# Optimization experiments

Measured on AMD Instinct MI355X. Metric: run time of the kernel, lower is better.

Reference implementation:

```python
import jax, jax.numpy as jnp
import numpy as np

TAU = 0.05       # sinkhorn temperature (functools.partial in GCN_Net)
SK_ITERS = 20    # sinkhorn max_iter


def _mlp(x, w1, b1, w2, b2):
    # nn.Sequential(Linear, ReLU, Linear)
    return jnp.maximum(x @ w1 + b1, 0.0) @ w2 + b2


def _cosine(f1, f2, eps=1e-8):
    # torch CosineSimilarity over broadcast (E1,1,D) x (1,E2,D), computed as a GEMM
    n1 = jnp.maximum(jnp.linalg.norm(f1, axis=-1), eps)
    n2 = jnp.maximum(jnp.linalg.norm(f2, axis=-1), eps)
    return (f1 @ f2.T) / (n1[:, None] * n2[None, :])


def _sinkhorn(s):
    # log-domain sinkhorn, alternating row/col normalization (pygmtools-style)
    log_s = s / TAU
    for i in range(SK_ITERS):
        log_s = log_s - jax.nn.logsumexp(log_s, axis=(1 if i % 2 == 0 else 0), keepdims=True)
    return jnp.exp(log_s)


def _build_conn_edges(preds):
    # fully-connected off-diagonal graph; edge feats [dx, dy, dist, cls_src, cls_dst]
    n = preds.shape[0]
    pos = preds[:, 1:3]
    cls = preds[:, 6]
    idx = np.arange(n)
    r, c = np.meshgrid(idx, idx, indexing='ij')
    m = r != c
    conn = np.stack([r[m], c[m]], axis=1)  # (E,2), static under jit
    src, dst = conn[:, 0], conn[:, 1]
    d = pos[dst] - pos[src]                             # (E,2)
    dist = jnp.linalg.norm(d, axis=-1, keepdims=True)   # (E,1)
    edges = jnp.concatenate([d, dist, cls[src][:, None], cls[dst][:, None]], axis=-1)  # (E,5)
    return jnp.asarray(conn), edges


def _forward(ego_preds, cav_preds, node_w1, node_b1, node_w2, node_b2,
             edge_w1, edge_b1, edge_w2, edge_b2,
             l0_self_w, l0_self_b, l0_conv_w, l0_conv_b, l0_cls_w, l0_cls_b,
             l1_self_w, l1_self_b, l1_conv_w, l1_conv_b, l1_cls_w, l1_cls_b,
             fc_w, fc_b):
    ego = ego_preds[0]
    cav = cav_preds[0]
    n1, n2 = ego.shape[0], cav.shape[0]
    conn1, e1 = _build_conn_edges(ego)
    conn2, e2 = _build_conn_edges(cav)
    # --- NodeMLP affinity ---
    f1 = _mlp(ego[:, 1:6], node_w1, node_b1, node_w2, node_b2)
    f2 = _mlp(cav[:, 1:6], node_w1, node_b1, node_w2, node_b2)
    cls_eq = (ego[:, 6][:, None] == cav[:, 6][None, :]).astype(ego.dtype)
    conf = jnp.sum(jnp.sqrt(ego[:, 7:][:, None, :] * cav[:, 7:][None, :, :]), axis=-1)
    node_aff = cls_eq * conf * _cosine(f1, f2)                         # (n1,n2)
    # --- EdgeMLP affinity ---
    g1 = _mlp(e1[:, :3], edge_w1, edge_b1, edge_w2, edge_b2)
    g2 = _mlp(e2[:, :3], edge_w1, edge_b1, edge_w2, edge_b2)
    ecls = jnp.all(e1[:, 3:].astype(jnp.int32)[:, None, :] == e2[:, 3:].astype(jnp.int32)[None, :, :],
                   axis=-1).astype(ego.dtype)
    edge_aff = ecls * _cosine(g1, g2)                                  # (E1,E2)
    # --- Lawler affinity matrix K over association graph: node (i,a) -> i*n2+a ---
    N = n1 * n2
    rows = (conn1[:, 0][:, None] * n2 + conn2[:, 0][None, :]).ravel()
    cols = (conn1[:, 1][:, None] * n2 + conn2[:, 1][None, :]).ravel()
    K = jnp.zeros((N, N), ego.dtype).at[rows, cols].set(edge_aff.ravel())
    d_idx = jnp.arange(N)
    K = K.at[d_idx, d_idx].set(node_aff.ravel())
    # --- GCN adjacency = nonzero pattern of K, with added self-loops + sym norm ---
    A = (K != 0).astype(ego.dtype) + jnp.eye(N, dtype=ego.dtype)
    dinv = jax.lax.rsqrt(A.sum(axis=1))
    normA = dinv[:, None] * A * dinv[None, :]
    x = jnp.diag(K)[:, None]                                           # (N,1)
    # --- NGMConvLayers: self-loop Linear + GCNConv + sinkhorn channel ---
    for sw, sb, cw, cb, kw, kb in (
            (l0_self_w, l0_self_b, l0_conv_w, l0_conv_b, l0_cls_w, l0_cls_b),
            (l1_self_w, l1_self_b, l1_conv_w, l1_conv_b, l1_cls_w, l1_cls_b)):
        x = (x @ sw + sb) + (normA @ (x @ cw) + cb)
        sk = _sinkhorn((x @ kw + kb).reshape(n1, n2))
        x = x + sk.reshape(-1, 1)
    scores = x @ fc_w + fc_b                                           # (N,1)
    s = scores.reshape(n2, n1).T                                       # view(n2,-1).t()
    return _sinkhorn(s)


def setup_inputs() -> dict:
    key = jax.random.key(0)
    ks = jax.random.split(key, 16)

    def lin(k, fi, fo):
        kw, kb = jax.random.split(k)
        s = (2.0 / (fi + fo)) ** 0.5
        return (jax.random.normal(kw, (fi, fo), jnp.float32) * s,
                jax.random.normal(kb, (fo,), jnp.float32) * 0.01)

    def make_preds(k, n):
        k1, k2 = jax.random.split(k)
        p = jax.random.uniform(k1, (1, n, 8), jnp.float32)
        cls = jnp.floor(jax.random.uniform(k2, (1, n)) * 3.0)  # 3 discrete classes
        p = p.at[:, :, 6].set(cls)
        p = p.at[:, :, 7].set(0.1 + 0.9 * p[:, :, 7])          # positive confidences
        return p

    inp = {'ego_preds': make_preds(ks[0], 64), 'cav_preds': make_preds(ks[1], 64)}
    inp['node_w1'], inp['node_b1'] = lin(ks[2], 5, 64)
    inp['node_w2'], inp['node_b2'] = lin(ks[3], 64, 32)
    inp['edge_w1'], inp['edge_b1'] = lin(ks[4], 3, 64)
    inp['edge_w2'], inp['edge_b2'] = lin(ks[5], 64, 32)
    inp['l0_self_w'], inp['l0_self_b'] = lin(ks[6], 1, 16)
    inp['l0_conv_w'], inp['l0_conv_b'] = lin(ks[7], 1, 16)
    inp['l0_cls_w'], inp['l0_cls_b'] = lin(ks[8], 16, 1)
    inp['l1_self_w'], inp['l1_self_b'] = lin(ks[9], 16, 16)
    inp['l1_conv_w'], inp['l1_conv_b'] = lin(ks[10], 16, 16)
    inp['l1_cls_w'], inp['l1_cls_b'] = lin(ks[11], 16, 1)
    inp['fc_w'], inp['fc_b'] = lin(ks[12], 16, 1)
    return inp


def reference(ego_preds, cav_preds, node_w1, node_b1, node_w2, node_b2,
              edge_w1, edge_b1, edge_w2, edge_b2,
              l0_self_w, l0_self_b, l0_conv_w, l0_conv_b, l0_cls_w, l0_cls_b,
              l1_self_w, l1_self_b, l1_conv_w, l1_conv_b, l1_cls_w, l1_cls_b,
              fc_w, fc_b):
    return _forward(ego_preds, cav_preds, node_w1, node_b1, node_w2, node_b2,
                    edge_w1, edge_b1, edge_w2, edge_b2,
                    l0_self_w, l0_self_b, l0_conv_w, l0_conv_b, l0_cls_w, l0_cls_b,
                    l1_self_w, l1_self_b, l1_conv_w, l1_conv_b, l1_cls_w, l1_cls_b,
                    fc_w, fc_b)
```

## Files before the change

kernel.cpp:

```cpp
#include <hip/hip_runtime.h>
#include <math.h>


#define TAU_INV 20.0f

template<int CTRL>
__device__ __forceinline__ float dppf(float x) {
    int xi = __float_as_int(x);
    int rr = __builtin_amdgcn_update_dpp(xi, xi, CTRL, 0xF, 0xF, false);
    return __int_as_float(rr);
}
__device__ __forceinline__ float red16_max(float v) {
    v = fmaxf(v, dppf<0xB1>(v));
    v = fmaxf(v, dppf<0x4E>(v));
    v = fmaxf(v, dppf<0x141>(v));
    v = fmaxf(v, dppf<0x140>(v));
    return v;
}
__device__ __forceinline__ float red16_sum(float v) {
    v += dppf<0xB1>(v);
    v += dppf<0x4E>(v);
    v += dppf<0x141>(v);
    v += dppf<0x140>(v);
    return v;
}
__device__ __forceinline__ float quad_sum(float v) {
    v += dppf<0xB1>(v);
    v += dppf<0x4E>(v);
    return v;
}
__device__ __forceinline__ float dot4(const float4 a, const float4 b) {
    return a.x*b.x + a.y*b.y + a.z*b.z + a.w*b.w;
}
__device__ __forceinline__ void fma4(float4& a, float b, const float4 c) {
    a.x += b*c.x; a.y += b*c.y; a.z += b*c.z; a.w += b*c.w;
}
__device__ __forceinline__ void add4(float4& a, const float4 c) {
    a.x += c.x; a.y += c.y; a.z += c.z; a.w += c.w;
}

__device__ void sinkhorn_rc(const float* tq, const float* tt, int tid, float* Rp, float* Cp) {
    const int g = tid >> 4, s = tid & 15;
    const int wa = 4 * (g & 15) + (g >> 4);
    for (int it = 0; it < 20; ++it) {
        if ((it & 1) == 0) {
            float4 cq = *(const float4*)(Cp + 4 * s);
            float z0 = tq[0]-cq.x, z1 = tq[1]-cq.y, z2 = tq[2]-cq.z, z3 = tq[3]-cq.w;
            float m  = red16_max(fmaxf(fmaxf(z0, z1), fmaxf(z2, z3)));
            float sm = red16_sum(__expf(z0-m) + __expf(z1-m) + __expf(z2-m) + __expf(z3-m));
            if (s == 0) Rp[wa] = __logf(sm) + m;
        } else {
            float4 rq = *(const float4*)(Rp + 4 * s);
            float z0 = tt[0]-rq.x, z1 = tt[1]-rq.y, z2 = tt[2]-rq.z, z3 = tt[3]-rq.w;
            float m  = red16_max(fmaxf(fmaxf(z0, z1), fmaxf(z2, z3)));
            float sm = red16_sum(__expf(z0-m) + __expf(z1-m) + __expf(z2-m) + __expf(z3-m));
            if (s == 0) Cp[wa] = __logf(sm) + m;
        }
        __syncthreads();
    }
}

__device__ void matvec_dual(const float* u1, const float* u2,
                            const float* mmq, const float* dq,
                            float* o1, float* o2, int tid,
                            float* WR1, float* WR2, float* WC1p, float* WC2p,
                            float* pwc, float* scW) {
    const int r = tid >> 4, s = tid & 15, lane = tid & 63, w = tid >> 6;
    float z1[4], z2[4];
    float rs1 = 0.0f, rs2 = 0.0f;
    #pragma unroll
    for (int k = 0; k < 4; ++k) {
        float md = mmq[k] * dq[k];
        z1[k] = md * u1[k];
        z2[k] = md * u2[k];
        rs1 += z1[k]; rs2 += z2[k];
    }
    rs1 = red16_sum(rs1); rs2 = red16_sum(rs2);
    if (s == 0) { WR1[r] = rs1; WR2[r] = rs2; }
    float p1[4], p2[4];
    #pragma unroll
    for (int k = 0; k < 4; ++k) {
        float v = z1[k]; v += __shfl_xor(v, 16); v += __shfl_xor(v, 32); p1[k] = v;
        float u = z2[k]; u += __shfl_xor(u, 16); u += __shfl_xor(u, 32); p2[k] = u;
    }
    if (lane < 16) {
        ((float4*)pwc)[w * 16 + s]          = make_float4(p1[0], p1[1], p1[2], p1[3]);
        ((float4*)(pwc + 1024))[w * 16 + s] = make_float4(p2[0], p2[1], p2[2], p2[3]);
    }
    __syncthreads();
    if (tid < 64) {
        float c1 = 0.0f, c2 = 0.0f;
        #pragma unroll
        for (int ww = 0; ww < 16; ++ww) {
            c1 += pwc[ww * 64 + tid];
            c2 += pwc[1024 + ww * 64 + tid];
        }
        WC1p[tid] = c1; WC2p[tid] = c2;
    } else if (tid < 128) {
        float v = WR1[tid - 64];
        #pragma unroll
        for (int off = 32; off > 0; off >>= 1) v += __shfl_xor(v, off);
        if (tid == 64) scW[0] = v;
    } else if (tid < 192) {
        float v = WR2[tid - 128];
        #pragma unroll
        for (int off = 32; off > 0; off >>= 1) v += __shfl_xor(v, off);
        if (tid == 128) scW[1] = v;
    }
    __syncthreads();
    const float W1 = scW[0], W2 = scW[1];
    const float wr1 = WR1[r], wr2 = WR2[r];
    float4 wc1 = *(const float4*)(WC1p + 4 * s);
    float4 wc2 = *(const float4*)(WC2p + 4 * s);
    const float wc1a[4] = {wc1.x, wc1.y, wc1.z, wc1.w};
    const float wc2a[4] = {wc2.x, wc2.y, wc2.z, wc2.w};
    #pragma unroll
    for (int k = 0; k < 4; ++k) {
        float d = dq[k], mm = mmq[k];
        o1[k] = d * ((1.0f + mm) * d * u1[k] + mm * (W1 - wr1 - wc1a[k] + z1[k]));
        o2[k] = d * ((1.0f + mm) * d * u2[k] + mm * (W2 - wr2 - wc2a[k] + z2[k]));
    }
    __syncthreads();
}

extern "C" __global__ __launch_bounds__(1024)
void gcn_match_kernel(const float* ego, const float* cav,
                      const float* nw1, const float* nb1, const float* nw2, const float* nb2,
                      const float* sw0, const float* sb0, const float* cw0, const float* cb0,
                      const float* kw0, const float* kb0,
                      const float* sw1, const float* sb1, const float* cw1, const float* cb1,
                      const float* kw1, const float* kb1,
                      const float* fcw, const float* fcb,
                      float* out) {
    __shared__ __align__(16) float sh_h1[64 * 68];
    __shared__ __align__(16) float sh_h2[64 * 68];
    __shared__ __align__(16) float sh_f1[64 * 36];
    __shared__ __align__(16) float sh_f2[64 * 36];
    __shared__ __align__(16) float sh_w2[2048];
    __shared__ __align__(16) float sh_nb2[32];
    __shared__ float sh_cls1[64], sh_cls2[64], sh_cf1[64], sh_cf2[64];
    __shared__ float sh_n1[64], sh_n2[64];
    __shared__ float sh_Dr[64], sh_Dc[64];
    __shared__ __align__(16) float sh_Rp[64], sh_Cp[64];
    __shared__ float sh_WR1[64], sh_WR2[64];
    __shared__ __align__(16) float sh_WC1p[64], sh_WC2p[64];
    __shared__ float sh_avec[7 * 16];
    __shared__ float sh_coef[18];
    __shared__ float sh_sc[4];

    const int tid  = threadIdx.x;
    const int wave = tid >> 6, lane = tid & 63;
    const int r = tid >> 4, s = tid & 15;

    if (tid < 512) ((float4*)sh_w2)[tid] = ((const float4*)nw2)[tid];
    if (tid < 32) sh_nb2[tid] = nb2[tid];
    if (tid < 64) { sh_cls1[tid] = ego[tid * 8 + 6]; sh_cf1[tid] = ego[tid * 8 + 7]; }
    else if (tid < 128) { int j = tid - 64; sh_cls2[j] = cav[j * 8 + 6]; sh_cf2[j] = cav[j * 8 + 7]; }
    {
        float w1r[5];
        #pragma unroll
        for (int f = 0; f < 5; ++f) w1r[f] = nw1[f * 64 + lane];
        float b1r = nb1[lane];
        #pragma unroll
        for (int p = 0; p < 4; ++p) {
            int i = wave + (p << 4);
            float4 e0 = ((const float4*)ego)[i * 2];
            float4 e1 = ((const float4*)ego)[i * 2 + 1];
            float a1 = b1r + e0.y*w1r[0] + e0.z*w1r[1] + e0.w*w1r[2] + e1.x*w1r[3] + e1.y*w1r[4];
            sh_h1[i * 68 + lane] = fmaxf(a1, 0.0f);
            float4 c0 = ((const float4*)cav)[i * 2];
            float4 c1 = ((const float4*)cav)[i * 2 + 1];
            float a2 = b1r + c0.y*w1r[0] + c0.z*w1r[1] + c0.w*w1r[2] + c1.x*w1r[3] + c1.y*w1r[4];
            sh_h2[i * 68 + lane] = fmaxf(a2, 0.0f);
        }
    }
    __syncthreads();

    if (wave < 4) {
        const int gw = wave & 1;
        const float* H = (wave < 2) ? sh_h1 : sh_h2;
        float* F  = (wave < 2) ? sh_f1 : sh_f2;
        float* NN = (wave < 2) ? sh_n1 : sh_n2;
        const int rr = lane >> 2, oq = lane & 3;
        const int i0 = 32 * gw + rr, i1 = i0 + 16;
        float4 a00 = make_float4(0,0,0,0), a01 = a00, a10 = a00, a11 = a00;
        #pragma unroll 4
        for (int k = 0; k < 64; ++k) {
            float  ha = H[i0 * 68 + k];
            float  hb = H[i1 * 68 + k];
            float4 wa = *(const float4*)(sh_w2 + k * 32 + 4 * oq);
            float4 wb = *(const float4*)(sh_w2 + k * 32 + 16 + 4 * oq);
            fma4(a00, ha, wa); fma4(a01, ha, wb);
            fma4(a10, hb, wa); fma4(a11, hb, wb);
        }
        float4 b2a = *(const float4*)(sh_nb2 + 4 * oq);
        float4 b2b = *(const float4*)(sh_nb2 + 16 + 4 * oq);
        add4(a00, b2a); add4(a01, b2b); add4(a10, b2a); add4(a11, b2b);
        *(float4*)(F + i0 * 36 + 4 * oq)      = a00;
        *(float4*)(F + i0 * 36 + 16 + 4 * oq) = a01;
        *(float4*)(F + i1 * 36 + 4 * oq)      = a10;
        *(float4*)(F + i1 * 36 + 16 + 4 * oq) = a11;
        float sq0 = quad_sum(dot4(a00, a00) + dot4(a01, a01));
        float sq1 = quad_sum(dot4(a10, a10) + dot4(a11, a11));
        if (oq == 0) {
            NN[i0] = fmaxf(sqrtf(sq0), 1e-8f);
            NN[i1] = fmaxf(sqrtf(sq1), 1e-8f);
        }
    } else if (wave == 4) {
        float c1v = sh_cls1[lane], d = 0.0f;
        for (int j = 0; j < 64; ++j) d += (c1v == sh_cls2[j]) ? 1.0f : 0.0f;
        sh_Dr[lane] = d;
        float t = d;
        #pragma unroll
        for (int off = 32; off > 0; off >>= 1) t += __shfl_xor(t, off);
        if (lane == 0) sh_sc[2] = t;
    } else if (wave == 5) {
        float c2v = sh_cls2[lane], d = 0.0f;
        for (int i = 0; i < 64; ++i) d += (sh_cls1[i] == c2v) ? 1.0f : 0.0f;
        sh_Dc[lane] = d;
    } else if (wave == 6 && lane < 16) {
        int o = lane;
        float ax = 0, av = 0, as_ = 0, aw = 0, au = 0, ae = 0, a1 = 0;
        for (int k = 0; k < 16; ++k) {
            float s0k = sw0[k], c0k = cw0[k], b0k = sb0[k] + cb0[k];
            float s1ko = sw1[k * 16 + o], c1ko = cw1[k * 16 + o];
            ax += s0k * s1ko;  av += c0k * s1ko + s0k * c1ko;  as_ += s1ko;
            aw += c0k * c1ko;  au += c1ko;  ae += b0k * c1ko;  a1 += b0k * s1ko;
        }
        a1 += sb1[o] + cb1[o];
        sh_avec[0*16+o] = ax; sh_avec[1*16+o] = av; sh_avec[2*16+o] = as_;
        sh_avec[3*16+o] = aw; sh_avec[4*16+o] = au; sh_avec[5*16+o] = ae;
        sh_avec[6*16+o] = a1;
    }
    __syncthreads();

    if (wave < 4) {
        const int sc = lane & 15, rc = lane >> 4;
        float dt[4][4];
        #pragma unroll
        for (int m = 0; m < 4; ++m)
            #pragma unroll
            for (int k = 0; k < 4; ++k) dt[m][k] = 0.0f;
        for (int kq = 0; kq < 8; ++kq) {
            float4 f2q[4];
            #pragma unroll
            for (int k = 0; k < 4; ++k)
                f2q[k] = *(const float4*)(sh_f2 + (sc + 16 * k) * 36 + 4 * kq);
            #pragma unroll
            for (int m = 0; m < 4; ++m) {
                int rrow = 16 * m + 4 * wave + rc;
                float4 f1q = *(const float4*)(sh_f1 + rrow * 36 + 4 * kq);
                #pragma unroll
                for (int k = 0; k < 4; ++k) dt[m][k] += dot4(f1q, f2q[k]);
            }
        }
        #pragma unroll
        for (int m = 0; m < 4; ++m) {
            int rrow = 16 * m + 4 * wave + rc;
            *(float4*)(sh_h1 + rrow * 68 + 4 * sc) =
                make_float4(dt[m][0], dt[m][1], dt[m][2], dt[m][3]);
        }
    } else if (wave == 4 && lane < 18) {
        int t = lane; float c = 0.0f;
        if (t == 0)      { for (int k = 0; k < 16; ++k) c += sw0[k] * kw0[k]; }
        else if (t == 1) { for (int k = 0; k < 16; ++k) c += cw0[k] * kw0[k]; }
        else if (t == 2) { for (int k = 0; k < 16; ++k) c += (sb0[k] + cb0[k]) * kw0[k]; c += kb0[0]; }
        else if (t < 10) { int v = t - 3;
            for (int o = 0; o < 16; ++o) c += sh_avec[v * 16 + o] * kw1[o];
            if (v == 6) c += kb1[0];
        } else if (t < 17) { int v = t - 10;
            for (int o = 0; o < 16; ++o) c += sh_avec[v * 16 + o] * fcw[o];
            if (v == 6) c += fcb[0];
        } else { for (int o = 0; o < 16; ++o) c += fcw[o]; }
        sh_coef[t] = c;
    } else if (wave == 5) {
        sh_Cp[lane] = 0.0f;
    }
    const float cls1r = sh_cls1[r];
    const float Tdeg = sh_sc[2], Drr = sh_Dr[r];
    const float n1r = sh_n1[r], cf1r = sh_cf1[r];
    float mmq[4], dqv[4], cfq[4], n2q[4];
    #pragma unroll
    for (int k = 0; k < 4; ++k) {
        int j = s + 16 * k;
        float mm = (cls1r == sh_cls2[j]) ? 1.0f : 0.0f;
        mmq[k] = mm;
        dqv[k] = (mm != 0.0f) ? (1.0f / sqrtf(Tdeg - Drr - sh_Dc[j] + 3.0f)) : 1.0f;
        cfq[k] = sqrtf(cf1r * sh_cf2[j]);
        n2q[k] = sh_n2[j];
    }
    __syncthreads();

    float x0[4];
    {
        float4 dq4 = *(const float4*)(sh_h1 + r * 68 + 4 * s);
        const float da[4] = {dq4.x, dq4.y, dq4.z, dq4.w};
        #pragma unroll
        for (int k = 0; k < 4; ++k)
            x0[k] = mmq[k] * cfq[k] * (da[k] / (n1r * n2q[k]));
    }
    __syncthreads();

    float v0[4], oe[4];
    {
        float ones[4] = {1.0f, 1.0f, 1.0f, 1.0f};
        matvec_dual(x0, ones, mmq, dqv, v0, oe, tid,
                    sh_WR1, sh_WR2, sh_WC1p, sh_WC2p, sh_h1, sh_sc);
    }

    const int pr = 4 * (r & 15) + (r >> 4);
    float t0q[4], t0t[4];
    {
        float c0 = sh_coef[0], c1 = sh_coef[1], c2 = sh_coef[2];
        #pragma unroll
        for (int k = 0; k < 4; ++k) t0q[k] = (c0 * x0[k] + c1 * v0[k] + c2) * TAU_INV;
    }
    *(float4*)(sh_h2 + r * 68 + 4 * s) = make_float4(t0q[0], t0q[1], t0q[2], t0q[3]);
    __syncthreads();
    #pragma unroll
    for (int k = 0; k < 4; ++k) t0t[k] = sh_h2[(s + 16 * k) * 68 + pr];
    sinkhorn_rc(t0q, t0t, tid, sh_Rp, sh_Cp);
    float s0[4];
    {
        float Rr = sh_Rp[pr];
        float4 cc = *(const float4*)(sh_Cp + 4 * s);
        const float ca[4] = {cc.x, cc.y, cc.z, cc.w};
        #pragma unroll
        for (int k = 0; k < 4; ++k) s0[k] = __expf(t0q[k] - Rr - ca[k]);
    }

    float ov[4], os[4];
    matvec_dual(v0, s0, mmq, dqv, ov, os, tid,
                sh_WR1, sh_WR2, sh_WC1p, sh_WC2p, sh_h1, sh_sc);
    float tacc[4], sacc[4];
    {
        float ctx = sh_coef[3], ctv = sh_coef[4], cts = sh_coef[5];
        float cw_ = sh_coef[6], cu_ = sh_coef[7], ce_ = sh_coef[8], ct1 = sh_coef[9];
        float csx = sh_coef[10], csv = sh_coef[11], css = sh_coef[12];
        float cw2 = sh_coef[13], cu2 = sh_coef[14], ce2 = sh_coef[15], cs1 = sh_coef[16];
        #pragma unroll
        for (int k = 0; k < 4; ++k) {
            tacc[k] = ctx * x0[k] + ctv * v0[k] + cts * s0[k] + ct1
                    + cw_ * ov[k] + cu_ * os[k] + ce_ * oe[k];
            sacc[k] = csx * x0[k] + csv * v0[k] + css * s0[k] + cs1
                    + cw2 * ov[k] + cu2 * os[k] + ce2 * oe[k];
        }
    }

    float t1q[4], t1t[4];
    #pragma unroll
    for (int k = 0; k < 4; ++k) t1q[k] = tacc[k] * TAU_INV;
    if (tid < 64) sh_Cp[tid] = 0.0f;
    *(float4*)(sh_h2 + r * 68 + 4 * s) = make_float4(t1q[0], t1q[1], t1q[2], t1q[3]);
    __syncthreads();
    #pragma unroll
    for (int k = 0; k < 4; ++k) t1t[k] = sh_h2[(s + 16 * k) * 68 + pr];
    sinkhorn_rc(t1q, t1t, tid, sh_Rp, sh_Cp);
    {
        float c17 = sh_coef[17];
        float Rr = sh_Rp[pr];
        float4 cc = *(const float4*)(sh_Cp + 4 * s);
        const float ca[4] = {cc.x, cc.y, cc.z, cc.w};
        #pragma unroll
        for (int k = 0; k < 4; ++k) sacc[k] += c17 * __expf(t1q[k] - Rr - ca[k]);
    }
    __syncthreads();

    if (tid < 64) sh_Cp[tid] = 0.0f;
    *(float4*)(sh_h2 + r * 68 + 4 * s) = make_float4(sacc[0], sacc[1], sacc[2], sacc[3]);
    __syncthreads();
    float t2q[4], t2t[4];
    #pragma unroll
    for (int k = 0; k < 4; ++k) {
        t2q[k] = sh_h2[(s + 16 * k) * 68 + pr] * TAU_INV;
        t2t[k] = sacc[k] * TAU_INV;
    }
    sinkhorn_rc(t2q, t2t, tid, sh_Rp, sh_Cp);
    {
        float Rr = sh_Rp[pr];
        float4 cc = *(const float4*)(sh_Cp + 4 * s);
        const float ca[4] = {cc.x, cc.y, cc.z, cc.w};
        #pragma unroll
        for (int k = 0; k < 4; ++k)
            out[r * 64 + s + 16 * k] = __expf(t2q[k] - Rr - ca[k]);
    }
}

extern "C" void kernel_launch(void* const* d_in, const int* in_sizes, int n_in,
                              void* d_out, int out_size, void* d_ws, size_t ws_size,
                              hipStream_t stream) {
    const float* ego = (const float*)d_in[0];
    const float* cav = (const float*)d_in[1];
    const float* nw1 = (const float*)d_in[2];
    const float* nb1 = (const float*)d_in[3];
    const float* nw2 = (const float*)d_in[4];
    const float* nb2 = (const float*)d_in[5];
    const float* sw0 = (const float*)d_in[10];
    const float* sb0 = (const float*)d_in[11];
    const float* cw0 = (const float*)d_in[12];
    const float* cb0 = (const float*)d_in[13];
    const float* kw0 = (const float*)d_in[14];
    const float* kb0 = (const float*)d_in[15];
    const float* sw1 = (const float*)d_in[16];
    const float* sb1 = (const float*)d_in[17];
    const float* cw1 = (const float*)d_in[18];
    const float* cb1 = (const float*)d_in[19];
    const float* kw1 = (const float*)d_in[20];
    const float* kb1 = (const float*)d_in[21];
    const float* fcw = (const float*)d_in[22];
    const float* fcb = (const float*)d_in[23];

    gcn_match_kernel<<<dim3(1), dim3(1024), 0, stream>>>(
        ego, cav, nw1, nb1, nw2, nb2,
        sw0, sb0, cw0, cb0, kw0, kb0,
        sw1, sb1, cw1, cb1, kw1, kb1,
        fcw, fcb, (float*)d_out);
}
```

Measured before the change: 136.5 us.

## Switch Sinkhorn to multiplicative scaling form and compute transposed tiles redundantly

```diff
diff --git a/kernel.cpp b/kernel.cpp
--- a/kernel.cpp
+++ b/kernel.cpp
@@ -2,7 +2,7 @@
 #include <math.h>
 
 
-#define TAU_INV 20.0f
+#define SK_SCALE 28.853900817779268f
 
 template<int CTRL>
 __device__ __forceinline__ float dppf(float x) {
@@ -18,17 +18,11 @@
     return v;
 }
 __device__ __forceinline__ float red16_sum(float v) {
-    v += dppf<0xB1>(v);
-    v += dppf<0x4E>(v);
-    v += dppf<0x141>(v);
-    v += dppf<0x140>(v);
+    v += dppf<0xB1>(v); v += dppf<0x4E>(v); v += dppf<0x141>(v); v += dppf<0x140>(v);
     return v;
 }
-__device__ __forceinline__ float quad_sum(float v) {
-    v += dppf<0xB1>(v);
-    v += dppf<0x4E>(v);
-    return v;
-}
+__device__ __forceinline__ float e2f(float x) { return __builtin_amdgcn_exp2f(x); }
+__device__ __forceinline__ float rcpf(float x) { return __builtin_amdgcn_rcpf(x); }
 __device__ __forceinline__ float dot4(const float4 a, const float4 b) {
     return a.x*b.x + a.y*b.y + a.z*b.z + a.w*b.w;
 }
@@ -38,89 +32,74 @@
 __device__ __forceinline__ void add4(float4& a, const float4 c) {
     a.x += c.x; a.y += c.y; a.z += c.z; a.w += c.w;
 }
-
-__device__ void sinkhorn_rc(const float* tq, const float* tt, int tid, float* Rp, float* Cp) {
-    const int g = tid >> 4, s = tid & 15;
-    const int wa = 4 * (g & 15) + (g >> 4);
-    for (int it = 0; it < 20; ++it) {
-        if ((it & 1) == 0) {
-            float4 cq = *(const float4*)(Cp + 4 * s);
-            float z0 = tq[0]-cq.x, z1 = tq[1]-cq.y, z2 = tq[2]-cq.z, z3 = tq[3]-cq.w;
-            float m  = red16_max(fmaxf(fmaxf(z0, z1), fmaxf(z2, z3)));
-            float sm = red16_sum(__expf(z0-m) + __expf(z1-m) + __expf(z2-m) + __expf(z3-m));
-            if (s == 0) Rp[wa] = __logf(sm) + m;
-        } else {
-            float4 rq = *(const float4*)(Rp + 4 * s);
-            float z0 = tt[0]-rq.x, z1 = tt[1]-rq.y, z2 = tt[2]-rq.z, z3 = tt[3]-rq.w;
-            float m  = red16_max(fmaxf(fmaxf(z0, z1), fmaxf(z2, z3)));
-            float sm = red16_sum(__expf(z0-m) + __expf(z1-m) + __expf(z2-m) + __expf(z3-m));
-            if (s == 0) Cp[wa] = __logf(sm) + m;
-        }
+__device__ __forceinline__ void ld4(const float* p, float* o) {
+    float4 v = *(const float4*)p; o[0]=v.x; o[1]=v.y; o[2]=v.z; o[3]=v.w;
+}
+
+__device__ void sk_mult(const float* tq, const float* tt, int s, int pr,
+                        float* up, float* vp, float* rmp,
+                        float* aq, float* att, float* u_out, float* v_out) {
+    float rm = red16_max(fmaxf(fmaxf(tq[0], tq[1]), fmaxf(tq[2], tq[3])));
+    #pragma unroll
+    for (int k = 0; k < 4; ++k) aq[k] = e2f(tq[k] - rm);
+    float u = rcpf(red16_sum(aq[0] + aq[1] + aq[2] + aq[3]));
+    if (s == 0) { rmp[pr] = rm; up[pr] = u; }
+    __syncthreads();
+    float rmq[4]; ld4(rmp + 4*s, rmq);
+    #pragma unroll
+    for (int k = 0; k < 4; ++k) att[k] = e2f(tt[k] - rmq[k]);
+    float v;
+    {
+        float uq[4]; ld4(up + 4*s, uq);
+        v = rcpf(red16_sum(att[0]*uq[0] + att[1]*uq[1] + att[2]*uq[2] + att[3]*uq[3]));
+        if (s == 0) vp[pr] = v;
         __syncthreads();
     }
-}
-
-__device__ void matvec_dual(const float* u1, const float* u2,
-                            const float* mmq, const float* dq,
-                            float* o1, float* o2, int tid,
-                            float* WR1, float* WR2, float* WC1p, float* WC2p,
-                            float* pwc, float* scW) {
-    const int r = tid >> 4, s = tid & 15, lane = tid & 63, w = tid >> 6;
-    float z1[4], z2[4];
-    float rs1 = 0.0f, rs2 = 0.0f;
+    #pragma unroll 1
+    for (int p = 0; p < 9; ++p) {
+        float vq[4]; ld4(vp + 4*s, vq);
+        u = rcpf(red16_sum(aq[0]*vq[0] + aq[1]*vq[1] + aq[2]*vq[2] + aq[3]*vq[3]));
+        if (s == 0) up[pr] = u;
+        __syncthreads();
+        float uq[4]; ld4(up + 4*s, uq);
+        v = rcpf(red16_sum(att[0]*uq[0] + att[1]*uq[1] + att[2]*uq[2] + att[3]*uq[3]));
+        if (s == 0) vp[pr] = v;
+        __syncthreads();
+    }
+    *u_out = u; *v_out = v;
+}
+
+__device__ void matvec_dual(const float* u1, const float* u1t, const float* u2, const float* u2t,
+                            const float* mmq, const float* dqv, const float* mmt, const float* dqt,
+                            float* o1, float* o1t, float* o2, float* o2t,
+                            int s, int pr,
+                            float* WR1p, float* WC1p, float* WR2p, float* WC2p) {
+    float z1[4], z2[4], z1t[4], z2t[4];
+    float rs1 = 0, rs2 = 0, cs1 = 0, cs2 = 0;
     #pragma unroll
     for (int k = 0; k < 4; ++k) {
-        float md = mmq[k] * dq[k];
-        z1[k] = md * u1[k];
-        z2[k] = md * u2[k];
-        rs1 += z1[k]; rs2 += z2[k];
+        float md = mmq[k] * dqv[k], mdt = mmt[k] * dqt[k];
+        z1[k] = md * u1[k];   z2[k] = md * u2[k];
+        z1t[k] = mdt * u1t[k]; z2t[k] = mdt * u2t[k];
+        rs1 += z1[k]; rs2 += z2[k]; cs1 += z1t[k]; cs2 += z2t[k];
     }
     rs1 = red16_sum(rs1); rs2 = red16_sum(rs2);
-    if (s == 0) { WR1[r] = rs1; WR2[r] = rs2; }
-    float p1[4], p2[4];
+    cs1 = red16_sum(cs1); cs2 = red16_sum(cs2);
+    if (s == 0) { WR1p[pr] = rs1; WR2p[pr] = rs2; WC1p[pr] = cs1; WC2p[pr] = cs2; }
+    __syncthreads();
+    float wr1[4], wc1[4], wr2[4], wc2[4];
+    ld4(WR1p + 4*s, wr1); ld4(WC1p + 4*s, wc1);
+    ld4(WR2p + 4*s, wr2); ld4(WC2p + 4*s, wc2);
+    float W1 = red16_sum(wc1[0] + wc1[1] + wc1[2] + wc1[3]);
+    float W2 = red16_sum(wc2[0] + wc2[1] + wc2[2] + wc2[3]);
     #pragma unroll
     for (int k = 0; k < 4; ++k) {
-        float v = z1[k]; v += __shfl_xor(v, 16); v += __shfl_xor(v, 32); p1[k] = v;
-        float u = z2[k]; u += __shfl_xor(u, 16); u += __shfl_xor(u, 32); p2[k] = u;
-    }
-    if (lane < 16) {
-        ((float4*)pwc)[w * 16 + s]          = make_float4(p1[0], p1[1], p1[2], p1[3]);
-        ((float4*)(pwc + 1024))[w * 16 + s] = make_float4(p2[0], p2[1], p2[2], p2[3]);
-    }
-    __syncthreads();
-    if (tid < 64) {
-        float c1 = 0.0f, c2 = 0.0f;
-        #pragma unroll
-        for (int ww = 0; ww < 16; ++ww) {
-            c1 += pwc[ww * 64 + tid];
-            c2 += pwc[1024 + ww * 64 + tid];
-        }
-        WC1p[tid] = c1; WC2p[tid] = c2;
-    } else if (tid < 128) {
-        float v = WR1[tid - 64];
-        #pragma unroll
-        for (int off = 32; off > 0; off >>= 1) v += __shfl_xor(v, off);
-        if (tid == 64) scW[0] = v;
-    } else if (tid < 192) {
-        float v = WR2[tid - 128];
-        #pragma unroll
-        for (int off = 32; off > 0; off >>= 1) v += __shfl_xor(v, off);
-        if (tid == 128) scW[1] = v;
-    }
-    __syncthreads();
-    const float W1 = scW[0], W2 = scW[1];
-    const float wr1 = WR1[r], wr2 = WR2[r];
-    float4 wc1 = *(const float4*)(WC1p + 4 * s);
-    float4 wc2 = *(const float4*)(WC2p + 4 * s);
-    const float wc1a[4] = {wc1.x, wc1.y, wc1.z, wc1.w};
-    const float wc2a[4] = {wc2.x, wc2.y, wc2.z, wc2.w};
-    #pragma unroll
-    for (int k = 0; k < 4; ++k) {
-        float d = dq[k], mm = mmq[k];
-        o1[k] = d * ((1.0f + mm) * d * u1[k] + mm * (W1 - wr1 - wc1a[k] + z1[k]));
-        o2[k] = d * ((1.0f + mm) * d * u2[k] + mm * (W2 - wr2 - wc2a[k] + z2[k]));
-    }
-    __syncthreads();
+        float d = dqv[k], mm = mmq[k], dt = dqt[k], mt = mmt[k];
+        o1[k]  = d  * ((1.0f + mm) * d  * u1[k]  + mm * (W1 - rs1 - wc1[k] + z1[k]));
+        o2[k]  = d  * ((1.0f + mm) * d  * u2[k]  + mm * (W2 - rs2 - wc2[k] + z2[k]));
+        o1t[k] = dt * ((1.0f + mt) * dt * u1t[k] + mt * (W1 - wr1[k] - cs1 + z1t[k]));
+        o2t[k] = dt * ((1.0f + mt) * dt * u2t[k] + mt * (W2 - wr2[k] - cs2 + z2t[k]));
+    }
 }
 
 extern "C" __global__ __launch_bounds__(1024)
@@ -132,93 +111,93 @@
                       const float* kw1, const float* kb1,
                       const float* fcw, const float* fcb,
                       float* out) {
-    __shared__ __align__(16) float sh_h1[64 * 68];
-    __shared__ __align__(16) float sh_h2[64 * 68];
+    __shared__ __align__(16) float sh_hT1[64 * 68];
+    __shared__ __align__(16) float sh_hT2[64 * 68];
+    __shared__ __align__(16) float sh_w2[2048];
     __shared__ __align__(16) float sh_f1[64 * 36];
     __shared__ __align__(16) float sh_f2[64 * 36];
-    __shared__ __align__(16) float sh_w2[2048];
     __shared__ __align__(16) float sh_nb2[32];
-    __shared__ float sh_cls1[64], sh_cls2[64], sh_cf1[64], sh_cf2[64];
-    __shared__ float sh_n1[64], sh_n2[64];
-    __shared__ float sh_Dr[64], sh_Dc[64];
-    __shared__ __align__(16) float sh_Rp[64], sh_Cp[64];
-    __shared__ float sh_WR1[64], sh_WR2[64];
-    __shared__ __align__(16) float sh_WC1p[64], sh_WC2p[64];
+    __shared__ float sh_cls1[64], sh_cf1[64], sh_n1[64];
+    __shared__ __align__(16) float sh_cls1p[64], sh_cf1p[64], sh_n1p[64];
+    __shared__ __align__(16) float sh_cls2p[64], sh_cf2p[64], sh_n2p[64];
+    __shared__ __align__(16) float sh_Drp[64], sh_Dcp[64];
+    __shared__ __align__(16) float sh_rmp[64], sh_up[64], sh_vp[64];
+    __shared__ __align__(16) float sh_WR1p[64], sh_WC1p[64], sh_WR2p[64], sh_WC2p[64];
     __shared__ float sh_avec[7 * 16];
     __shared__ float sh_coef[18];
-    __shared__ float sh_sc[4];
 
     const int tid  = threadIdx.x;
     const int wave = tid >> 6, lane = tid & 63;
     const int r = tid >> 4, s = tid & 15;
+    const int pr = 4 * (r & 15) + (r >> 4);
+    float* sh_dots = sh_hT1;
 
     if (tid < 512) ((float4*)sh_w2)[tid] = ((const float4*)nw2)[tid];
     if (tid < 32) sh_nb2[tid] = nb2[tid];
-    if (tid < 64) { sh_cls1[tid] = ego[tid * 8 + 6]; sh_cf1[tid] = ego[tid * 8 + 7]; }
-    else if (tid < 128) { int j = tid - 64; sh_cls2[j] = cav[j * 8 + 6]; sh_cf2[j] = cav[j * 8 + 7]; }
-    {
-        float w1r[5];
-        #pragma unroll
-        for (int f = 0; f < 5; ++f) w1r[f] = nw1[f * 64 + lane];
-        float b1r = nb1[lane];
-        #pragma unroll
-        for (int p = 0; p < 4; ++p) {
-            int i = wave + (p << 4);
-            float4 e0 = ((const float4*)ego)[i * 2];
-            float4 e1 = ((const float4*)ego)[i * 2 + 1];
-            float a1 = b1r + e0.y*w1r[0] + e0.z*w1r[1] + e0.w*w1r[2] + e1.x*w1r[3] + e1.y*w1r[4];
-            sh_h1[i * 68 + lane] = fmaxf(a1, 0.0f);
-            float4 c0 = ((const float4*)cav)[i * 2];
-            float4 c1 = ((const float4*)cav)[i * 2 + 1];
-            float a2 = b1r + c0.y*w1r[0] + c0.z*w1r[1] + c0.w*w1r[2] + c1.x*w1r[3] + c1.y*w1r[4];
-            sh_h2[i * 68 + lane] = fmaxf(a2, 0.0f);
-        }
-    }
-    __syncthreads();
-
-    if (wave < 4) {
-        const int gw = wave & 1;
-        const float* H = (wave < 2) ? sh_h1 : sh_h2;
-        float* F  = (wave < 2) ? sh_f1 : sh_f2;
-        float* NN = (wave < 2) ? sh_n1 : sh_n2;
+    if (tid < 64) {
+        float c = ego[tid * 8 + 6], f = ego[tid * 8 + 7];
+        int p = 4 * (tid & 15) + (tid >> 4);
+        sh_cls1[tid] = c; sh_cf1[tid] = f; sh_cls1p[p] = c; sh_cf1p[p] = f;
+    } else if (tid < 128) {
+        int j = tid - 64, p = 4 * (j & 15) + (j >> 4);
+        sh_cls2p[p] = cav[j * 8 + 6]; sh_cf2p[p] = cav[j * 8 + 7];
+    }
+    {
+        const float* X = (wave < 8) ? ego : cav;
+        float* HT = (wave < 8) ? sh_hT1 : sh_hT2;
+        const int k0 = (wave & 7) * 8;
+        float4 xa = ((const float4*)X)[lane * 2];
+        float4 xb = ((const float4*)X)[lane * 2 + 1];
+        #pragma unroll
+        for (int kk = 0; kk < 8; ++kk) {
+            int k = k0 + kk;
+            float acc = nb1[k] + xa.y * nw1[k] + xa.z * nw1[64 + k] + xa.w * nw1[128 + k]
+                      + xb.x * nw1[192 + k] + xb.y * nw1[256 + k];
+            HT[k * 68 + lane] = fmaxf(acc, 0.0f);
+        }
+    }
+    __syncthreads();
+
+    if (wave < 2) {
+        const float* HT = (wave == 0) ? sh_hT1 : sh_hT2;
+        float* F = (wave == 0) ? sh_f1 : sh_f2;
         const int rr = lane >> 2, oq = lane & 3;
-        const int i0 = 32 * gw + rr, i1 = i0 + 16;
-        float4 a00 = make_float4(0,0,0,0), a01 = a00, a10 = a00, a11 = a00;
+        float4 accA[4], accB[4];
+        #pragma unroll
+        for (int m = 0; m < 4; ++m) { accA[m] = make_float4(0,0,0,0); accB[m] = accA[m]; }
         #pragma unroll 4
         for (int k = 0; k < 64; ++k) {
-            float  ha = H[i0 * 68 + k];
-            float  hb = H[i1 * 68 + k];
-            float4 wa = *(const float4*)(sh_w2 + k * 32 + 4 * oq);
-            float4 wb = *(const float4*)(sh_w2 + k * 32 + 16 + 4 * oq);
-            fma4(a00, ha, wa); fma4(a01, ha, wb);
-            fma4(a10, hb, wa); fma4(a11, hb, wb);
+            float4 hq = *(const float4*)(HT + k * 68 + 4 * rr);
+            float4 wA = *(const float4*)(sh_w2 + k * 32 + 4 * oq);
+            float4 wB = *(const float4*)(sh_w2 + k * 32 + 16 + 4 * oq);
+            fma4(accA[0], hq.x, wA); fma4(accB[0], hq.x, wB);
+            fma4(accA[1], hq.y, wA); fma4(accB[1], hq.y, wB);
+            fma4(accA[2], hq.z, wA); fma4(accB[2], hq.z, wB);
+            fma4(accA[3], hq.w, wA); fma4(accB[3], hq.w, wB);
         }
         float4 b2a = *(const float4*)(sh_nb2 + 4 * oq);
         float4 b2b = *(const float4*)(sh_nb2 + 16 + 4 * oq);
-        add4(a00, b2a); add4(a01, b2b); add4(a10, b2a); add4(a11, b2b);
-        *(float4*)(F + i0 * 36 + 4 * oq)      = a00;
-        *(float4*)(F + i0 * 36 + 16 + 4 * oq) = a01;
-        *(float4*)(F + i1 * 36 + 4 * oq)      = a10;
-        *(float4*)(F + i1 * 36 + 16 + 4 * oq) = a11;
-        float sq0 = quad_sum(dot4(a00, a00) + dot4(a01, a01));
-        float sq1 = quad_sum(dot4(a10, a10) + dot4(a11, a11));
+        float sq[4];
+        #pragma unroll
+        for (int m = 0; m < 4; ++m) {
+            add4(accA[m], b2a); add4(accB[m], b2b);
+            int row = 4 * rr + m;
+            *(float4*)(F + row * 36 + 4 * oq)      = accA[m];
+            *(float4*)(F + row * 36 + 16 + 4 * oq) = accB[m];
+            float q = dot4(accA[m], accA[m]) + dot4(accB[m], accB[m]);
+            q += dppf<0xB1>(q); q += dppf<0x4E>(q);
+            sq[m] = q;
+        }
         if (oq == 0) {
-            NN[i0] = fmaxf(sqrtf(sq0), 1e-8f);
-            NN[i1] = fmaxf(sqrtf(sq1), 1e-8f);
-        }
-    } else if (wave == 4) {
-        float c1v = sh_cls1[lane], d = 0.0f;
-        for (int j = 0; j < 64; ++j) d += (c1v == sh_cls2[j]) ? 1.0f : 0.0f;
-        sh_Dr[lane] = d;
-        float t = d;
-        #pragma unroll
-        for (int off = 32; off > 0; off >>= 1) t += __shfl_xor(t, off);
-        if (lane == 0) sh_sc[2] = t;
-    } else if (wave == 5) {
-        float c2v = sh_cls2[lane], d = 0.0f;
-        for (int i = 0; i < 64; ++i) d += (sh_cls1[i] == c2v) ? 1.0f : 0.0f;
-        sh_Dc[lane] = d;
-    } else if (wave == 6 && lane < 16) {
+            #pragma unroll
+            for (int m = 0; m < 4; ++m) {
+                int row = 4 * rr + m, p = 4 * (row & 15) + (row >> 4);
+                float n = fmaxf(sqrtf(sq[m]), 1e-8f);
+                if (wave == 0) { sh_n1[row] = n; sh_n1p[p] = n; }
+                else           { sh_n2p[p] = n; }
+            }
+        }
+    } else if (wave == 2 && lane < 16) {
         int o = lane;
         float ax = 0, av = 0, as_ = 0, aw = 0, au = 0, ae = 0, a1 = 0;
         for (int k = 0; k < 16; ++k) {
@@ -257,7 +236,7 @@
         #pragma unroll
         for (int m = 0; m < 4; ++m) {
             int rrow = 16 * m + 4 * wave + rc;
-            *(float4*)(sh_h1 + rrow * 68 + 4 * sc) =
+            *(float4*)(sh_dots + rrow * 68 + 4 * sc) =
                 make_float4(dt[m][0], dt[m][1], dt[m][2], dt[m][3]);
         }
     } else if (wave == 4 && lane < 18) {
@@ -273,66 +252,79 @@
             if (v == 6) c += fcb[0];
         } else { for (int o = 0; o < 16; ++o) c += fcw[o]; }
         sh_coef[t] = c;
-    } else if (wave == 5) {
-        sh_Cp[lane] = 0.0f;
-    }
-    const float cls1r = sh_cls1[r];
-    const float Tdeg = sh_sc[2], Drr = sh_Dr[r];
-    const float n1r = sh_n1[r], cf1r = sh_cf1[r];
-    float mmq[4], dqv[4], cfq[4], n2q[4];
-    #pragma unroll
-    for (int k = 0; k < 4; ++k) {
-        int j = s + 16 * k;
-        float mm = (cls1r == sh_cls2[j]) ? 1.0f : 0.0f;
-        mmq[k] = mm;
-        dqv[k] = (mm != 0.0f) ? (1.0f / sqrtf(Tdeg - Drr - sh_Dc[j] + 3.0f)) : 1.0f;
-        cfq[k] = sqrtf(cf1r * sh_cf2[j]);
-        n2q[k] = sh_n2[j];
-    }
-    __syncthreads();
-
-    float x0[4];
-    {
-        float4 dq4 = *(const float4*)(sh_h1 + r * 68 + 4 * s);
-        const float da[4] = {dq4.x, dq4.y, dq4.z, dq4.w};
-        #pragma unroll
-        for (int k = 0; k < 4; ++k)
-            x0[k] = mmq[k] * cfq[k] * (da[k] / (n1r * n2q[k]));
-    }
-    __syncthreads();
-
-    float v0[4], oe[4];
+    }
+    float mmq[4], mmt[4], cfq[4], cft[4];
+    float Drr, Dcr;
+    {
+        const float cls1r = sh_cls1[r], cls2r = sh_cls2p[pr];
+        const float cf1r = sh_cf1[r],  cf2r  = sh_cf2p[pr];
+        float c2q[4], c1q[4], f2q[4], f1q[4];
+        ld4(sh_cls2p + 4*s, c2q); ld4(sh_cls1p + 4*s, c1q);
+        ld4(sh_cf2p + 4*s, f2q);  ld4(sh_cf1p + 4*s, f1q);
+        float dr = 0, dc = 0;
+        #pragma unroll
+        for (int k = 0; k < 4; ++k) {
+            mmq[k] = (cls1r == c2q[k]) ? 1.0f : 0.0f;
+            mmt[k] = (c1q[k] == cls2r) ? 1.0f : 0.0f;
+            dr += mmq[k]; dc += mmt[k];
+            cfq[k] = sqrtf(cf1r * f2q[k]);
+            cft[k] = sqrtf(f1q[k] * cf2r);
+        }
+        Drr = red16_sum(dr);
+        Dcr = red16_sum(dc);
+        if (s == 0) { sh_Drp[pr] = Drr; sh_Dcp[pr] = Dcr; }
+    }
+    __syncthreads();
+
+    float dqv[4], dqt[4], x0[4], x0t[4];
+    {
+        float dcq[4], drq[4], n2q[4], n1q[4], dotq[4];
+        ld4(sh_Dcp + 4*s, dcq); ld4(sh_Drp + 4*s, drq);
+        ld4(sh_n2p + 4*s, n2q); ld4(sh_n1p + 4*s, n1q);
+        ld4(sh_dots + r * 68 + 4*s, dotq);
+        float Tdeg = red16_sum(dcq[0] + dcq[1] + dcq[2] + dcq[3]);
+        const float n1r = sh_n1[r], n2r = sh_n2p[pr];
+        #pragma unroll
+        for (int k = 0; k < 4; ++k) {
+            dqv[k] = (mmq[k] != 0.0f) ? (1.0f / sqrtf(Tdeg - Drr - dcq[k] + 3.0f)) : 1.0f;
+            dqt[k] = (mmt[k] != 0.0f) ? (1.0f / sqrtf(Tdeg - drq[k] - Dcr + 3.0f)) : 1.0f;
+            x0[k] = mmq[k] * cfq[k] * (dotq[k] / (n1r * n2q[k]));
+            float dott = sh_dots[(s + 16 * k) * 68 + pr];
+            x0t[k] = mmt[k] * cft[k] * (dott / (n1q[k] * n2r));
+        }
+    }
+
+    float v0[4], v0t[4], oe[4], oet[4];
     {
         float ones[4] = {1.0f, 1.0f, 1.0f, 1.0f};
-        matvec_dual(x0, ones, mmq, dqv, v0, oe, tid,
-                    sh_WR1, sh_WR2, sh_WC1p, sh_WC2p, sh_h1, sh_sc);
-    }
-
-    const int pr = 4 * (r & 15) + (r >> 4);
-    float t0q[4], t0t[4];
+        matvec_dual(x0, x0t, ones, ones, mmq, dqv, mmt, dqt,
+                    v0, v0t, oe, oet, s, pr, sh_WR1p, sh_WC1p, sh_WR2p, sh_WC2p);
+    }
+
+    float aq[4], att[4], u0, vv0;
+    float s0[4], s0t[4];
     {
         float c0 = sh_coef[0], c1 = sh_coef[1], c2 = sh_coef[2];
-        #pragma unroll
-        for (int k = 0; k < 4; ++k) t0q[k] = (c0 * x0[k] + c1 * v0[k] + c2) * TAU_INV;
-    }
-    *(float4*)(sh_h2 + r * 68 + 4 * s) = make_float4(t0q[0], t0q[1], t0q[2], t0q[3]);
-    __syncthreads();
-    #pragma unroll
-    for (int k = 0; k < 4; ++k) t0t[k] = sh_h2[(s + 16 * k) * 68 + pr];
-    sinkhorn_rc(t0q, t0t, tid, sh_Rp, sh_Cp);
-    float s0[4];
-    {
-        float Rr = sh_Rp[pr];
-        float4 cc = *(const float4*)(sh_Cp + 4 * s);
-        const float ca[4] = {cc.x, cc.y, cc.z, cc.w};
-        #pragma unroll
-        for (int k = 0; k < 4; ++k) s0[k] = __expf(t0q[k] - Rr - ca[k]);
-    }
-
-    float ov[4], os[4];
-    matvec_dual(v0, s0, mmq, dqv, ov, os, tid,
-                sh_WR1, sh_WR2, sh_WC1p, sh_WC2p, sh_h1, sh_sc);
-    float tacc[4], sacc[4];
+        float t0q[4], t0t[4];
+        #pragma unroll
+        for (int k = 0; k < 4; ++k) {
+            t0q[k] = (c0 * x0[k]  + c1 * v0[k]  + c2) * SK_SCALE;
+            t0t[k] = (c0 * x0t[k] + c1 * v0t[k] + c2) * SK_SCALE;
+        }
+        sk_mult(t0q, t0t, s, pr, sh_up, sh_vp, sh_rmp, aq, att, &u0, &vv0);
+        float vq[4], uq[4];
+        ld4(sh_vp + 4*s, vq); ld4(sh_up + 4*s, uq);
+        #pragma unroll
+        for (int k = 0; k < 4; ++k) {
+            s0[k]  = aq[k] * u0 * vq[k];
+            s0t[k] = att[k] * uq[k] * vv0;
+        }
+    }
+
+    float ov[4], ovt[4], os[4], ost[4];
+    matvec_dual(v0, v0t, s0, s0t, mmq, dqv, mmt, dqt,
+                ov, ovt, os, ost, s, pr, sh_WR1p, sh_WC1p, sh_WR2p, sh_WC2p);
+    float t1q[4], t1t[4], sacc[4], sacct[4];
     {
         float ctx = sh_coef[3], ctv = sh_coef[4], cts = sh_coef[5];
         float cw_ = sh_coef[6], cu_ = sh_coef[7], ce_ = sh_coef[8], ct1 = sh_coef[9];
@@ -340,49 +332,44 @@
         float cw2 = sh_coef[13], cu2 = sh_coef[14], ce2 = sh_coef[15], cs1 = sh_coef[16];
         #pragma unroll
         for (int k = 0; k < 4; ++k) {
-            tacc[k] = ctx * x0[k] + ctv * v0[k] + cts * s0[k] + ct1
-                    + cw_ * ov[k] + cu_ * os[k] + ce_ * oe[k];
+            t1q[k] = (ctx * x0[k] + ctv * v0[k] + cts * s0[k] + ct1
+                    + cw_ * ov[k] + cu_ * os[k] + ce_ * oe[k]) * SK_SCALE;
+            t1t[k] = (ctx * x0t[k] + ctv * v0t[k] + cts * s0t[k] + ct1
+                    + cw_ * ovt[k] + cu_ * ost[k] + ce_ * oet[k]) * SK_SCALE;
             sacc[k] = csx * x0[k] + csv * v0[k] + css * s0[k] + cs1
                     + cw2 * ov[k] + cu2 * os[k] + ce2 * oe[k];
-        }
-    }
-
-    float t1q[4], t1t[4];
-    #pragma unroll
-    for (int k = 0; k < 4; ++k) t1q[k] = tacc[k] * TAU_INV;
-    if (tid < 64) sh_Cp[tid] = 0.0f;
-    *(float4*)(sh_h2 + r * 68 + 4 * s) = make_float4(t1q[0], t1q[1], t1q[2], t1q[3]);
-    __syncthreads();
-    #pragma unroll
-    for (int k = 0; k < 4; ++k) t1t[k] = sh_h2[(s + 16 * k) * 68 + pr];
-    sinkhorn_rc(t1q, t1t, tid, sh_Rp, sh_Cp);
-    {
+            sacct[k] = csx * x0t[k] + csv * v0t[k] + css * s0t[k] + cs1
+                    + cw2 * ovt[k] + cu2 * ost[k] + ce2 * oet[k];
+        }
+    }
+
+    {
+        float u1, v1;
+        sk_mult(t1q, t1t, s, pr, sh_up, sh_vp, sh_rmp, aq, att, &u1, &v1);
         float c17 = sh_coef[17];
-        float Rr = sh_Rp[pr];
-        float4 cc = *(const float4*)(sh_Cp + 4 * s);
-        const float ca[4] = {cc.x, cc.y, cc.z, cc.w};
-        #pragma unroll
-        for (int k = 0; k < 4; ++k) sacc[k] += c17 * __expf(t1q[k] - Rr - ca[k]);
-    }
-    __syncthreads();
-
-    if (tid < 64) sh_Cp[tid] = 0.0f;
-    *(float4*)(sh_h2 + r * 68 + 4 * s) = make_float4(sacc[0], sacc[1], sacc[2], sacc[3]);
-    __syncthreads();
-    float t2q[4], t2t[4];
-    #pragma unroll
-    for (int k = 0; k < 4; ++k) {
-        t2q[k] = sh_h2[(s + 16 * k) * 68 + pr] * TAU_INV;
-        t2t[k] = sacc[k] * TAU_INV;
-    }
-    sinkhorn_rc(t2q, t2t, tid, sh_Rp, sh_Cp);
-    {
-        float Rr = sh_Rp[pr];
-        float4 cc = *(const float4*)(sh_Cp + 4 * s);
-        const float ca[4] = {cc.x, cc.y, cc.z, cc.w};
+        float vq[4], uq[4];
+        ld4(sh_vp + 4*s, vq); ld4(sh_up + 4*s, uq);
+        #pragma unroll
+        for (int k = 0; k < 4; ++k) {
+            sacc[k]  += c17 * aq[k] * u1 * vq[k];
+            sacct[k] += c17 * att[k] * uq[k] * v1;
+        }
+    }
+    __syncthreads();
+
+    {
+        float t2q[4], t2t[4];
+        #pragma unroll
+        for (int k = 0; k < 4; ++k) {
+            t2q[k] = sacct[k] * SK_SCALE;
+            t2t[k] = sacc[k] * SK_SCALE;
+        }
+        float u2, v2;
+        sk_mult(t2q, t2t, s, pr, sh_up, sh_vp, sh_rmp, aq, att, &u2, &v2);
+        float vq[4]; ld4(sh_vp + 4*s, vq);
         #pragma unroll
         for (int k = 0; k < 4; ++k)
-            out[r * 64 + s + 16 * k] = __expf(t2q[k] - Rr - ca[k]);
+            out[(r << 6) + s + (k << 4)] = aq[k] * u2 * vq[k];
     }
 }
 
```

New measurement: 123.9 us. 1.1x faster.
